# Optimization experiments

Measured on AMD Instinct MI355X. Metric: run time of the kernel, lower is better.

Reference implementation:

```python
import jax, jax.numpy as jnp
import numpy as np

G, L, NSTA, NSRC, K = 10000, 1000, 400, 2000, 15
SIG = 10.0
FTRNS_SCALE = 1000.0  # ftrns1_diff(x) = x * 1000 (km -> m style linear transform)
FUDGE = 1.0


def setup_inputs() -> dict:
    key = jax.random.key(0)
    ks = jax.random.split(key, 9)
    sta = 10.0 * jax.random.normal(ks[0], (NSTA, 3), jnp.float32)
    src = 10.0 * jax.random.normal(ks[1], (NSRC, 3), jnp.float32)
    mag = jax.random.normal(ks[2], (NSRC,), jnp.float32)
    phase = jax.random.randint(ks[3], (NSTA,), 0, 2)
    x_grid = 10.0 * jax.random.normal(ks[4], (G, 3), jnp.float32)
    locs_ref = 10.0 * jax.random.normal(ks[5], (L, 3), jnp.float32)
    mag_coef = jnp.ones(2, jnp.float32)
    epicenter_spatial_coef = jnp.ones(2, jnp.float32)
    depth_spatial_coef = 0.1 * jax.random.normal(ks[6], (2,), jnp.float32)
    coefs = 0.1 * jax.random.normal(ks[7], (G, L, 2), jnp.float32)
    coefs_ker = SIG + 0.1 * jax.random.normal(ks[8], (G, L, 3), jnp.float32)
    return {"sta": sta, "src": src, "mag": mag, "phase": phase,
            "x_grid": x_grid, "locs_ref": locs_ref, "mag_coef": mag_coef,
            "epicenter_spatial_coef": epicenter_spatial_coef,
            "depth_spatial_coef": depth_spatial_coef,
            "coefs": coefs, "coefs_ker": coefs_ker}


def _ftrns(x):
    return x * FTRNS_SCALE


def _magnitude_fwd(sta, src, mag, phase, x_grid, locs_ref, mag_coef,
                   epicenter_spatial_coef, depth_spatial_coef, coefs, coefs_ker):
    sp = jax.nn.softplus
    zvec = jnp.array([1.0, 1.0, 0.0], dtype=sta.dtype)

    # nearest reference station index for each station (knn k=1)
    locs_ref_cart = _ftrns(locs_ref) / 1000.0            # [L,3]
    sta_pos = _ftrns(sta) / 1000.0                       # [Nsta,3]
    d2_ref = ((sta_pos[:, None, :] - locs_ref_cart[None, :, :]) ** 2).sum(-1)
    sta_ind = jnp.argmin(d2_ref, axis=1)                 # [Nsta]

    # pairwise log-distance matrices [Nsrc, Nsta]
    pw_log_dist_zero = jnp.log10(
        jnp.linalg.norm(_ftrns(src * zvec)[:, None, :] - _ftrns(sta * zvec)[None, :, :], axis=2) + FUDGE)
    pw_log_dist_depths = jnp.log10(jnp.abs(src[:, 2][:, None] - sta[:, 2][None, :]) + FUDGE)

    # --- anisotropic kNN interpolation of coefs[:, sta_ind, :] from grid to src ---
    pos1 = _ftrns(x_grid) / 1000.0                       # [G,3]
    pos2 = _ftrns(src) / 1000.0                          # [Nsrc,3]
    dq = ((pos2[:, None, :] - pos1[None, :, :]) ** 2).sum(-1)  # [Nsrc,G]
    _, idx = jax.lax.top_k(-dq, K)                       # [Nsrc,K] nearest grid nodes

    coefs_sub = coefs[:, sta_ind, :]                     # [G,Nsta,2]
    ker_sub = coefs_ker[:, sta_ind, :]                   # [G,Nsta,3]

    diff = pos1[idx] - pos2[:, None, :]                  # [Nsrc,K,3]
    ker_e = sp(ker_sub[idx])                             # [Nsrc,K,Nsta,3]
    w = jnp.exp(-0.5 * ((diff[:, :, None, :] / ker_e) ** 2).sum(-1))  # [Nsrc,K,Nsta]
    wsum = w.sum(axis=1, keepdims=True)                  # [Nsrc,1,Nsta]
    wsum = jnp.where(wsum == 0.0, 1.0, wsum)
    w = w / wsum
    bias_l = jnp.einsum('qkn,qknc->qnc', w, coefs_sub[idx])  # [Nsrc,Nsta,2]

    # phase-selected bias and coefficients
    bias = jnp.where(phase[None, :] == 0, bias_l[:, :, 0], bias_l[:, :, 1])  # [Nsrc,Nsta]
    mc = sp(mag_coef)[phase]                             # [Nsta]
    ec = sp(epicenter_spatial_coef)[phase]
    dc = depth_spatial_coef[phase]

    log_amp = (mag[:, None] * mc[None, :]
               - ec[None, :] * pw_log_dist_zero
               + dc[None, :] * pw_log_dist_depths
               + bias)                                   # [Nsrc,Nsta]
    return log_amp


def reference(sta, src, mag, phase, x_grid, locs_ref, mag_coef,
              epicenter_spatial_coef, depth_spatial_coef, coefs, coefs_ker):
    return _magnitude_fwd(sta, src, mag, phase, x_grid, locs_ref, mag_coef,
                          epicenter_spatial_coef, depth_spatial_coef, coefs, coefs_ker)
```

## Files before the change

### kernel.cpp

```cpp
#include <hip/hip_runtime.h>
#include <hip/hip_fp16.h>
#include <cstddef>

#define G_N   10000
#define L_N   1000
#define NSTA  400
#define NSRC  2000
#define KK    15
#define CAP   512

__device__ __forceinline__ float tr1k(float x) {
    return (x * 1000.0f) / 1000.0f;
}

__device__ __forceinline__ float softplus(float x) {
    return fmaxf(x, 0.0f) + log1pf(expf(-fabsf(x)));
}

__device__ __forceinline__ float softplus_fast(float x) {
    return fmaxf(x, 0.0f) + __logf(1.0f + __expf(-fabsf(x)));
}

__device__ __forceinline__ bool lexless(float v1, int i1, float v2, int i2) {
    return (v1 < v2) || (v1 == v2 && i1 < i2);
}

__global__ void sta_prep_kernel(const float* __restrict__ sta,
                                const float* __restrict__ locs_ref,
                                const float* __restrict__ x_grid,
                                const float* __restrict__ src,
                                int* __restrict__ sta_ind,
                                float* __restrict__ tg,
                                float* __restrict__ ts,
                                int* __restrict__ used) {
#pragma clang fp contract(off)
    const int i    = blockIdx.x;
    const int lane = threadIdx.x;

    const int z = i * 64 + lane;
    for (int p = z; p < 3 * (G_N + NSRC); p += 400 * 64) {
        if (p < 3 * G_N) tg[p] = tr1k(x_grid[p]);
        else             ts[p - 3 * G_N] = tr1k(src[p - 3 * G_N]);
    }
    if (used && z < G_N) used[z] = 0;

    const float sx = tr1k(sta[i * 3 + 0]);
    const float sy = tr1k(sta[i * 3 + 1]);
    const float sz = tr1k(sta[i * 3 + 2]);
    float best = INFINITY;
    int   bidx = 0x7fffffff;
    for (int j = lane; j < L_N; j += 64) {
        float dx = sx - tr1k(locs_ref[j * 3 + 0]);
        float dy = sy - tr1k(locs_ref[j * 3 + 1]);
        float dz = sz - tr1k(locs_ref[j * 3 + 2]);
        float d  = (dx * dx + dy * dy) + dz * dz;
        if (lexless(d, j, best, bidx)) { best = d; bidx = j; }
    }
    for (int off = 1; off < 64; off <<= 1) {
        float ov = __shfl_xor(best, off);
        int   oi = __shfl_xor(bidx, off);
        if (lexless(ov, oi, best, bidx)) { best = ov; bidx = oi; }
    }
    if (lane == 0) sta_ind[i] = bidx;
}

__global__ __launch_bounds__(256, 8) void topk_only_kernel(
    const float* __restrict__ tg, const float* __restrict__ ts,
    int* __restrict__ idx_out, int* __restrict__ used)
{
#pragma clang fp contract(off)
    const int s    = blockIdx.x;
    const int tid  = threadIdx.x;
    const int lane = tid & 63;
    const int wv   = tid >> 6;

    __shared__ float s_min[256];
    __shared__ int   s_cand[CAP];
    __shared__ float s_cd[CAP];
    __shared__ float s_T;
    __shared__ int   s_cnt;
    __shared__ float s_mv[4];
    __shared__ int   s_mi[4];
    __shared__ int   s_ch[KK];

    if (tid == 0) s_cnt = 0;

    const float sx = ts[s * 3 + 0];
    const float sy = ts[s * 3 + 1];
    const float sz = ts[s * 3 + 2];

    float mymin = INFINITY;
    for (int g = tid; g < G_N; g += 256) {
        float dx = sx - tg[g * 3 + 0];
        float dy = sy - tg[g * 3 + 1];
        float dz = sz - tg[g * 3 + 2];
        float d  = (dx * dx + dy * dy) + dz * dz;
        mymin = fminf(mymin, d);
    }
    s_min[tid] = mymin;
    __syncthreads();

    if (wv == 0) {
        float m0 = s_min[lane];
        float m1 = s_min[lane + 64];
        float m2 = s_min[lane + 128];
        float m3 = s_min[lane + 192];
        float T = INFINITY;
        for (int r = 0; r < KK; ++r) {
            float lv = m0; int ls = 0;
            if (m1 < lv) { lv = m1; ls = 1; }
            if (m2 < lv) { lv = m2; ls = 2; }
            if (m3 < lv) { lv = m3; ls = 3; }
            float v = lv; int wl = lane;
            for (int off = 1; off < 64; off <<= 1) {
                float ov = __shfl_xor(v, off);
                int   ol = __shfl_xor(wl, off);
                if (ov < v || (ov == v && ol < wl)) { v = ov; wl = ol; }
            }
            T = v;
            if (wl == lane) {
                if (ls == 0) m0 = INFINITY;
                else if (ls == 1) m1 = INFINITY;
                else if (ls == 2) m2 = INFINITY;
                else m3 = INFINITY;
            }
        }
        if (lane == 0) s_T = T;
    }
    __syncthreads();
    const float T = s_T;

    for (int g = tid; g < G_N; g += 256) {
        float dx = sx - tg[g * 3 + 0];
        float dy = sy - tg[g * 3 + 1];
        float dz = sz - tg[g * 3 + 2];
        float d  = (dx * dx + dy * dy) + dz * dz;
        if (d <= T) {
            int p = atomicAdd(&s_cnt, 1);
            if (p < CAP) { s_cand[p] = g; s_cd[p] = d; }
        }
    }
    __syncthreads();
    const int n = s_cnt;

    if (n <= CAP) {
        if (wv == 0) {
            float vals[KK];
            int   ids[KK];
#pragma unroll
            for (int j = 0; j < KK; ++j) { vals[j] = INFINITY; ids[j] = 0x7fffffff; }
            for (int c = lane; c < n; c += 64) {
                int   g = s_cand[c];
                float d = s_cd[c];
                if (lexless(d, g, vals[KK - 1], ids[KK - 1])) {
                    float cv = d; int ci = g;
#pragma unroll
                    for (int j = 0; j < KK; ++j) {
                        bool sw = lexless(cv, ci, vals[j], ids[j]);
                        float tv = sw ? vals[j] : cv;
                        int   ti = sw ? ids[j]  : ci;
                        vals[j]  = sw ? cv : vals[j];
                        ids[j]   = sw ? ci : ids[j];
                        cv = tv; ci = ti;
                    }
                }
            }
            for (int r = 0; r < KK; ++r) {
                float v  = vals[0];
                int   id = ids[0];
                int   who = lane;
                for (int off = 1; off < 64; off <<= 1) {
                    float ov = __shfl_xor(v, off);
                    int   oi = __shfl_xor(id, off);
                    int   ow = __shfl_xor(who, off);
                    if (lexless(ov, oi, v, id)) { v = ov; id = oi; who = ow; }
                }
                if (lane == 0) {
                    idx_out[s * KK + r] = id;
                    if (used) used[id] = 1;
                }
                if (who == lane) {
#pragma unroll
                    for (int j = 0; j < KK - 1; ++j) { vals[j] = vals[j + 1]; ids[j] = ids[j + 1]; }
                    vals[KK - 1] = INFINITY;
                    ids[KK - 1]  = 0x7fffffff;
                }
            }
        }
    } else {
        for (int r = 0; r < KK; ++r) {
            float v  = INFINITY;
            int   id = 0x7fffffff;
            for (int g = tid; g < G_N; g += 256) {
                bool skip = false;
                for (int j = 0; j < r; ++j) skip = skip || (s_ch[j] == g);
                if (skip) continue;
                float dx = sx - tg[g * 3 + 0];
                float dy = sy - tg[g * 3 + 1];
                float dz = sz - tg[g * 3 + 2];
                float d  = (dx * dx + dy * dy) + dz * dz;
                if (lexless(d, g, v, id)) { v = d; id = g; }
            }
            for (int off = 1; off < 64; off <<= 1) {
                float ov = __shfl_xor(v, off);
                int   oi = __shfl_xor(id, off);
                if (lexless(ov, oi, v, id)) { v = ov; id = oi; }
            }
            if (lane == 0) { s_mv[wv] = v; s_mi[wv] = id; }
            __syncthreads();
            if (tid == 0) {
                float bv = s_mv[0]; int bi = s_mi[0];
                for (int w = 1; w < 4; ++w)
                    if (lexless(s_mv[w], s_mi[w], bv, bi)) { bv = s_mv[w]; bi = s_mi[w]; }
                s_ch[r] = bi;
                idx_out[s * KK + r] = bi;
                if (used) used[bi] = 1;
            }
            __syncthreads();
        }
    }
}

__global__ __launch_bounds__(256, 8) void pack_kernel(
    const float* __restrict__ coefs, const float* __restrict__ coefs_ker,
    const int* __restrict__ sta_ind, const int* __restrict__ phase,
    const int* __restrict__ used,
    uint2* __restrict__ pk)
{
    const int g = blockIdx.x;
    if (!used[g]) return;
    const int tid  = threadIdx.x;
    const int lane = tid & 63;
    const int wv   = tid >> 6;

    __shared__ __align__(16) float s_all[5120];

    const float4* kr4 = (const float4*)(coefs_ker + (size_t)g * (L_N * 3));
    const float4* cr4 = (const float4*)(coefs     + (size_t)g * (L_N * 2));

#pragma unroll
    for (int r = 0; r < 5; ++r) {
        const int chunk = wv * 5 + r;
        const int slot  = chunk * 64 + lane;
        const float4* gp = (slot < 750) ? (kr4 + slot)
                         : (slot < 1250) ? (cr4 + (slot - 750))
                         : (cr4 + 499);
        __builtin_amdgcn_global_load_lds(
            (const __attribute__((address_space(1))) void*)gp,
            (__attribute__((address_space(3))) void*)(s_all + (size_t)chunk * 256),
            16, 0, 0);
    }

    const int i1  = tid + 256;
    const int st0 = sta_ind[tid];
    const int ph0 = phase[tid];
    const int st1 = (i1 < NSTA) ? sta_ind[i1] : 0;
    const int ph1 = (i1 < NSTA) ? phase[i1] : 0;
    __syncthreads();

    const float* s_ker = s_all;
    const float* s_c   = s_all + 3000;

    {
        float rk0 = 1.0f / softplus_fast(s_ker[st0 * 3 + 0]);
        float rk1 = 1.0f / softplus_fast(s_ker[st0 * 3 + 1]);
        float rk2 = 1.0f / softplus_fast(s_ker[st0 * 3 + 2]);
        float c   = (ph0 == 0) ? s_c[st0 * 2 + 0] : s_c[st0 * 2 + 1];
        __half2 a = __floats2half2_rn(rk0, rk1);
        __half2 b = __floats2half2_rn(rk2, c);
        uint2 u;
        u.x = *reinterpret_cast<unsigned int*>(&a);
        u.y = *reinterpret_cast<unsigned int*>(&b);
        pk[(size_t)g * NSTA + tid] = u;
    }
    if (i1 < NSTA) {
        float rk0 = 1.0f / softplus_fast(s_ker[st1 * 3 + 0]);
        float rk1 = 1.0f / softplus_fast(s_ker[st1 * 3 + 1]);
        float rk2 = 1.0f / softplus_fast(s_ker[st1 * 3 + 2]);
        float c   = (ph1 == 0) ? s_c[st1 * 2 + 0] : s_c[st1 * 2 + 1];
        __half2 a = __floats2half2_rn(rk0, rk1);
        __half2 b = __floats2half2_rn(rk2, c);
        uint2 u;
        u.x = *reinterpret_cast<unsigned int*>(&a);
        u.y = *reinterpret_cast<unsigned int*>(&b);
        pk[(size_t)g * NSTA + i1] = u;
    }
}

__global__ __launch_bounds__(256, 8) void magnitude_fast_kernel(
    const float* __restrict__ sta, const float* __restrict__ src,
    const float* __restrict__ mag, const int* __restrict__ phase,
    const float* __restrict__ x_grid,
    const float* __restrict__ mag_coef, const float* __restrict__ epi_coef,
    const float* __restrict__ dep_coef,
    const uint2* __restrict__ pk, const int* __restrict__ idx,
    float* __restrict__ out)
{
    const int s   = blockIdx.x;
    const int tid = threadIdx.x;

    __shared__ float s_diff[KK][3];
    __shared__ int   s_g[KK];

    if (tid < KK) {
        int g = idx[s * KK + tid];
        s_g[tid] = g;
        s_diff[tid][0] = tr1k(x_grid[g * 3 + 0]) - tr1k(src[s * 3 + 0]);
        s_diff[tid][1] = tr1k(x_grid[g * 3 + 1]) - tr1k(src[s * 3 + 1]);
        s_diff[tid][2] = tr1k(x_grid[g * 3 + 2]) - tr1k(src[s * 3 + 2]);
    }
    __syncthreads();

    const float mag_s = mag[s];
    const float srcx = src[s * 3 + 0];
    const float srcy = src[s * 3 + 1];
    const float srcz = src[s * 3 + 2];
    const float sp_mc0 = softplus(mag_coef[0]), sp_mc1 = softplus(mag_coef[1]);
    const float sp_ec0 = softplus(epi_coef[0]), sp_ec1 = softplus(epi_coef[1]);
    const float dc0 = dep_coef[0], dc1 = dep_coef[1];

    for (int i = tid; i < NSTA; i += 256) {
        float wsum = 0.0f, a = 0.0f;
#pragma unroll
        for (int k = 0; k < KK; ++k) {
            uint2 u = pk[(size_t)s_g[k] * NSTA + i];
            __half2 h01 = *reinterpret_cast<const __half2*>(&u.x);
            __half2 h23 = *reinterpret_cast<const __half2*>(&u.y);
            float2 f01 = __half22float2(h01);
            float2 f23 = __half22float2(h23);
            float t0 = s_diff[k][0] * f01.x;
            float t1 = s_diff[k][1] * f01.y;
            float t2 = s_diff[k][2] * f23.x;
            float e  = __expf(-0.5f * ((t0 * t0 + t1 * t1) + t2 * t2));
            wsum += e;
            a    += e * f23.y;
        }
        if (wsum == 0.0f) wsum = 1.0f;

        const int ph = phase[i];
        float bias = a / wsum;

        float dx = srcx * 1000.0f - sta[i * 3 + 0] * 1000.0f;
        float dy = srcy * 1000.0f - sta[i * 3 + 1] * 1000.0f;
        float lz = __log10f(__fsqrt_rn(dx * dx + dy * dy) + 1.0f);
        float ld = __log10f(fabsf(srcz - sta[i * 3 + 2]) + 1.0f);

        float mc = (ph == 0) ? sp_mc0 : sp_mc1;
        float ec = (ph == 0) ? sp_ec0 : sp_ec1;
        float dc = (ph == 0) ? dc0 : dc1;

        out[(size_t)s * NSTA + i] = mag_s * mc - ec * lz + dc * ld + bias;
    }
}

__global__ __launch_bounds__(256) void magnitude_kernel(
    const float* __restrict__ sta, const float* __restrict__ src,
    const float* __restrict__ mag, const int* __restrict__ phase,
    const float* __restrict__ x_grid,
    const float* __restrict__ mag_coef, const float* __restrict__ epi_coef,
    const float* __restrict__ dep_coef,
    const float* __restrict__ coefs, const float* __restrict__ coefs_ker,
    const int* __restrict__ sta_ind, const int* __restrict__ idx,
    float* __restrict__ out)
{
    const int s   = blockIdx.x;
    const int tid = threadIdx.x;

    __shared__ float s_diff[KK][3];
    __shared__ int   s_g[KK];
    __shared__ int   s_sta[NSTA];

    if (tid < KK) {
        int g = idx[s * KK + tid];
        s_g[tid] = g;
        s_diff[tid][0] = tr1k(x_grid[g * 3 + 0]) - tr1k(src[s * 3 + 0]);
        s_diff[tid][1] = tr1k(x_grid[g * 3 + 1]) - tr1k(src[s * 3 + 1]);
        s_diff[tid][2] = tr1k(x_grid[g * 3 + 2]) - tr1k(src[s * 3 + 2]);
    }
    for (int i = tid; i < NSTA; i += 256) s_sta[i] = sta_ind[i];
    __syncthreads();

    const float mag_s = mag[s];
    const float srcx = src[s * 3 + 0];
    const float srcy = src[s * 3 + 1];
    const float srcz = src[s * 3 + 2];
    const float sp_mc0 = softplus(mag_coef[0]), sp_mc1 = softplus(mag_coef[1]);
    const float sp_ec0 = softplus(epi_coef[0]), sp_ec1 = softplus(epi_coef[1]);
    const float dc0 = dep_coef[0], dc1 = dep_coef[1];

    for (int i = tid; i < NSTA; i += 256) {
        const int st = s_sta[i];
        float wsum = 0.0f, a0 = 0.0f, a1 = 0.0f;
#pragma unroll
        for (int k = 0; k < KK; ++k) {
            const int g = s_g[k];
            const float* kp = coefs_ker + ((size_t)g * L_N + st) * 3;
            float k0 = softplus(kp[0]);
            float k1 = softplus(kp[1]);
            float k2 = softplus(kp[2]);
            float t0 = s_diff[k][0] / k0;
            float t1 = s_diff[k][1] / k1;
            float t2 = s_diff[k][2] / k2;
            float e  = expf(-0.5f * ((t0 * t0 + t1 * t1) + t2 * t2));
            const float* cp = coefs + ((size_t)g * L_N + st) * 2;
            wsum += e;
            a0 += e * cp[0];
            a1 += e * cp[1];
        }
        if (wsum == 0.0f) wsum = 1.0f;

        const int ph = phase[i];
        float bias = ((ph == 0) ? a0 : a1) / wsum;

        float dx = srcx * 1000.0f - sta[i * 3 + 0] * 1000.0f;
        float dy = srcy * 1000.0f - sta[i * 3 + 1] * 1000.0f;
        float lz = log10f(sqrtf(dx * dx + dy * dy) + 1.0f);
        float ld = log10f(fabsf(srcz - sta[i * 3 + 2]) + 1.0f);

        float mc = (ph == 0) ? sp_mc0 : sp_mc1;
        float ec = (ph == 0) ? sp_ec0 : sp_ec1;
        float dc = (ph == 0) ? dc0 : dc1;

        out[(size_t)s * NSTA + i] = mag_s * mc - ec * lz + dc * ld + bias;
    }
}

extern "C" void kernel_launch(void* const* d_in, const int* in_sizes, int n_in,
                              void* d_out, int out_size, void* d_ws, size_t ws_size,
                              hipStream_t stream) {
    const float* sta       = (const float*)d_in[0];
    const float* src       = (const float*)d_in[1];
    const float* mag       = (const float*)d_in[2];
    const int*   phase     = (const int*)d_in[3];
    const float* x_grid    = (const float*)d_in[4];
    const float* locs_ref  = (const float*)d_in[5];
    const float* mag_coef  = (const float*)d_in[6];
    const float* epi_coef  = (const float*)d_in[7];
    const float* dep_coef  = (const float*)d_in[8];
    const float* coefs     = (const float*)d_in[9];
    const float* coefs_ker = (const float*)d_in[10];
    float* out = (float*)d_out;

    const size_t pk_bytes = (size_t)G_N * NSTA * sizeof(uint2);
    const size_t tail_ints = (size_t)NSRC * KK + NSTA + G_N + 3 * G_N + 3 * NSRC;
    const size_t need_fast = pk_bytes + tail_ints * 4;

    if (ws_size >= need_fast) {
        uint2* ws_pk   = (uint2*)d_ws;
        int*   ws_idx  = (int*)((char*)d_ws + pk_bytes);
        int*   ws_sta  = ws_idx + (size_t)NSRC * KK;
        int*   ws_used = ws_sta + NSTA;
        float* ws_tg   = (float*)(ws_used + G_N);
        float* ws_ts   = ws_tg + 3 * G_N;

        hipLaunchKernelGGL(sta_prep_kernel, dim3(NSTA), dim3(64), 0, stream,
                           sta, locs_ref, x_grid, src, ws_sta, ws_tg, ws_ts, ws_used);
        hipLaunchKernelGGL(topk_only_kernel, dim3(NSRC), dim3(256), 0, stream,
                           ws_tg, ws_ts, ws_idx, ws_used);
        hipLaunchKernelGGL(pack_kernel, dim3(G_N), dim3(256), 0, stream,
                           coefs, coefs_ker, ws_sta, phase, ws_used, ws_pk);
        hipLaunchKernelGGL(magnitude_fast_kernel, dim3(NSRC), dim3(256), 0, stream,
                           sta, src, mag, phase, x_grid,
                           mag_coef, epi_coef, dep_coef,
                           ws_pk, ws_idx, out);
    } else {
        int*   ws_sta  = (int*)d_ws;
        int*   ws_idx  = ws_sta + NSTA;
        float* ws_tg   = (float*)(ws_idx + (size_t)NSRC * KK);
        float* ws_ts   = ws_tg + 3 * G_N;

        hipLaunchKernelGGL(sta_prep_kernel, dim3(NSTA), dim3(64), 0, stream,
                           sta, locs_ref, x_grid, src, ws_sta, ws_tg, ws_ts, (int*)nullptr);
        hipLaunchKernelGGL(topk_only_kernel, dim3(NSRC), dim3(256), 0, stream,
                           ws_tg, ws_ts, ws_idx, (int*)nullptr);
        hipLaunchKernelGGL(magnitude_kernel, dim3(NSRC), dim3(256), 0, stream,
                           sta, src, mag, phase, x_grid,
                           mag_coef, epi_coef, dep_coef,
                           coefs, coefs_ker, ws_sta, ws_idx, out);
    }
}
```

Before: 122.4 us.

## Make pack kernel persistent over grid rows with double-buffered LDS staging

```diff
diff --git a/kernel.cpp b/kernel.cpp
--- a/kernel.cpp
+++ b/kernel.cpp
@@ -8,6 +8,7 @@
 #define NSRC  2000
 #define KK    15
 #define CAP   512
+#define NBLK  1250
 
 __device__ __forceinline__ float tr1k(float x) {
     return (x * 1000.0f) / 1000.0f;
@@ -221,69 +222,94 @@
     }
 }
 
-__global__ __launch_bounds__(256, 8) void pack_kernel(
+__global__ __launch_bounds__(256) void pack_kernel(
     const float* __restrict__ coefs, const float* __restrict__ coefs_ker,
     const int* __restrict__ sta_ind, const int* __restrict__ phase,
     const int* __restrict__ used,
     uint2* __restrict__ pk)
 {
-    const int g = blockIdx.x;
-    if (!used[g]) return;
+    __shared__ __align__(16) float s_buf[2][5120];
+    __shared__ int s_list[8];
+    __shared__ int s_n;
+
     const int tid  = threadIdx.x;
     const int lane = tid & 63;
     const int wv   = tid >> 6;
 
-    __shared__ __align__(16) float s_all[5120];
-
-    const float4* kr4 = (const float4*)(coefs_ker + (size_t)g * (L_N * 3));
-    const float4* cr4 = (const float4*)(coefs     + (size_t)g * (L_N * 2));
-
-#pragma unroll
-    for (int r = 0; r < 5; ++r) {
-        const int chunk = wv * 5 + r;
-        const int slot  = chunk * 64 + lane;
-        const float4* gp = (slot < 750) ? (kr4 + slot)
-                         : (slot < 1250) ? (cr4 + (slot - 750))
-                         : (cr4 + 499);
-        __builtin_amdgcn_global_load_lds(
-            (const __attribute__((address_space(1))) void*)gp,
-            (__attribute__((address_space(3))) void*)(s_all + (size_t)chunk * 256),
-            16, 0, 0);
-    }
+    if (tid == 0) {
+        int n = 0;
+        for (int r = blockIdx.x; r < G_N; r += NBLK)
+            if (used[r]) s_list[n++] = r;
+        s_n = n;
+    }
+    __syncthreads();
+    const int n = s_n;
+    if (n == 0) return;
 
     const int i1  = tid + 256;
     const int st0 = sta_ind[tid];
     const int ph0 = phase[tid];
     const int st1 = (i1 < NSTA) ? sta_ind[i1] : 0;
     const int ph1 = (i1 < NSTA) ? phase[i1] : 0;
-    __syncthreads();
-
-    const float* s_ker = s_all;
-    const float* s_c   = s_all + 3000;
-
-    {
-        float rk0 = 1.0f / softplus_fast(s_ker[st0 * 3 + 0]);
-        float rk1 = 1.0f / softplus_fast(s_ker[st0 * 3 + 1]);
-        float rk2 = 1.0f / softplus_fast(s_ker[st0 * 3 + 2]);
-        float c   = (ph0 == 0) ? s_c[st0 * 2 + 0] : s_c[st0 * 2 + 1];
-        __half2 a = __floats2half2_rn(rk0, rk1);
-        __half2 b = __floats2half2_rn(rk2, c);
-        uint2 u;
-        u.x = *reinterpret_cast<unsigned int*>(&a);
-        u.y = *reinterpret_cast<unsigned int*>(&b);
-        pk[(size_t)g * NSTA + tid] = u;
-    }
-    if (i1 < NSTA) {
-        float rk0 = 1.0f / softplus_fast(s_ker[st1 * 3 + 0]);
-        float rk1 = 1.0f / softplus_fast(s_ker[st1 * 3 + 1]);
-        float rk2 = 1.0f / softplus_fast(s_ker[st1 * 3 + 2]);
-        float c   = (ph1 == 0) ? s_c[st1 * 2 + 0] : s_c[st1 * 2 + 1];
-        __half2 a = __floats2half2_rn(rk0, rk1);
-        __half2 b = __floats2half2_rn(rk2, c);
-        uint2 u;
-        u.x = *reinterpret_cast<unsigned int*>(&a);
-        u.y = *reinterpret_cast<unsigned int*>(&b);
-        pk[(size_t)g * NSTA + i1] = u;
+
+    auto stage = [&](int buf, int row) {
+        const float4* kr4 = (const float4*)(coefs_ker + (size_t)row * (L_N * 3));
+        const float4* cr4 = (const float4*)(coefs     + (size_t)row * (L_N * 2));
+#pragma unroll
+        for (int r = 0; r < 5; ++r) {
+            const int chunk = wv * 5 + r;
+            const int slot  = chunk * 64 + lane;
+            const float4* gp = (slot < 750) ? (kr4 + slot)
+                             : (slot < 1250) ? (cr4 + (slot - 750))
+                             : (cr4 + 499);
+            __builtin_amdgcn_global_load_lds(
+                (const __attribute__((address_space(1))) void*)gp,
+                (__attribute__((address_space(3))) void*)(&s_buf[buf][0] + (size_t)chunk * 256),
+                16, 0, 0);
+        }
+    };
+
+    stage(0, s_list[0]);
+    for (int r = 0; r < n; ++r) {
+        const int cur = r & 1;
+        if (r + 1 < n) {
+            stage(cur ^ 1, s_list[r + 1]);
+            asm volatile("s_waitcnt vmcnt(5)" ::: "memory");
+        } else {
+            asm volatile("s_waitcnt vmcnt(0)" ::: "memory");
+        }
+        __builtin_amdgcn_s_barrier();
+        __builtin_amdgcn_sched_barrier(0);
+
+        const float* s_ker = &s_buf[cur][0];
+        const float* s_c   = &s_buf[cur][3000];
+        const int g = s_list[r];
+
+        {
+            float rk0 = 1.0f / softplus_fast(s_ker[st0 * 3 + 0]);
+            float rk1 = 1.0f / softplus_fast(s_ker[st0 * 3 + 1]);
+            float rk2 = 1.0f / softplus_fast(s_ker[st0 * 3 + 2]);
+            float c   = (ph0 == 0) ? s_c[st0 * 2 + 0] : s_c[st0 * 2 + 1];
+            __half2 a = __floats2half2_rn(rk0, rk1);
+            __half2 b = __floats2half2_rn(rk2, c);
+            uint2 u;
+            u.x = *reinterpret_cast<unsigned int*>(&a);
+            u.y = *reinterpret_cast<unsigned int*>(&b);
+            pk[(size_t)g * NSTA + tid] = u;
+        }
+        if (i1 < NSTA) {
+            float rk0 = 1.0f / softplus_fast(s_ker[st1 * 3 + 0]);
+            float rk1 = 1.0f / softplus_fast(s_ker[st1 * 3 + 1]);
+            float rk2 = 1.0f / softplus_fast(s_ker[st1 * 3 + 2]);
+            float c   = (ph1 == 0) ? s_c[st1 * 2 + 0] : s_c[st1 * 2 + 1];
+            __half2 a = __floats2half2_rn(rk0, rk1);
+            __half2 b = __floats2half2_rn(rk2, c);
+            uint2 u;
+            u.x = *reinterpret_cast<unsigned int*>(&a);
+            u.y = *reinterpret_cast<unsigned int*>(&b);
+            pk[(size_t)g * NSTA + i1] = u;
+        }
+        __builtin_amdgcn_s_barrier();
     }
 }
 
@@ -457,7 +483,7 @@
                            sta, locs_ref, x_grid, src, ws_sta, ws_tg, ws_ts, ws_used);
         hipLaunchKernelGGL(topk_only_kernel, dim3(NSRC), dim3(256), 0, stream,
                            ws_tg, ws_ts, ws_idx, ws_used);
-        hipLaunchKernelGGL(pack_kernel, dim3(G_N), dim3(256), 0, stream,
+        hipLaunchKernelGGL(pack_kernel, dim3(NBLK), dim3(256), 0, stream,
                            coefs, coefs_ker, ws_sta, phase, ws_used, ws_pk);
         hipLaunchKernelGGL(magnitude_fast_kernel, dim3(NSRC), dim3(256), 0, stream,
                            sta, src, mag, phase, x_grid,
```

Measured after the change: 128.8 us. 5.2% more time.
